# Optimization experiments

Hardware: AMD Instinct MI355X
Metric: run time of the kernel (lower is better)

Reference implementation:

```python
import jax, jax.numpy as jnp
import numpy as np

GAMMA = 1.0

def _rbf_mean(X, Y, gamma):
    x2 = jnp.sum(X * X, axis=1)  # [n]
    y2 = jnp.sum(Y * Y, axis=1)  # [m]
    d2 = x2[:, None] + y2[None, :] - 2.0 * (X @ Y.T)
    d2 = jnp.maximum(d2, 0.0)
    return jnp.mean(jnp.exp(-gamma * d2))

def setup_inputs() -> dict:
    key = jax.random.key(0)
    k1, k2 = jax.random.split(key)
    N = jax.random.normal(k1, (8192, 256), dtype=jnp.float32)
    R = jax.random.normal(k2, (8192, 256), dtype=jnp.float32)
    return {"N": N, "R": R}

def reference(N, R):
    xx = _rbf_mean(N, N, GAMMA)
    yy = _rbf_mean(R, R, GAMMA)
    xy = _rbf_mean(N, R, GAMMA)
    mmd = xx + yy - 2.0 * xy
    return jnp.sqrt(mmd)
```

## Files before the change

### kernel.cpp

```cpp
#include <hip/hip_runtime.h>
#include <math.h>

typedef float f32x4 __attribute__((ext_vector_type(4)));
typedef int   i32x4 __attribute__((ext_vector_type(4)));
typedef int   i32x8 __attribute__((ext_vector_type(8)));
typedef float f32x2 __attribute__((ext_vector_type(2)));

#define MTOT 16384
#define HALF 8192
#define KDIM 256
#define BM 128
#define NB (MTOT / BM)
#define NBLK (NB * (NB + 1) / 2)
#define NPART (NBLK * 4)

#define GLDS16(g, l) __builtin_amdgcn_global_load_lds(                      \
    (const __attribute__((address_space(1))) void*)(g),                     \
    (__attribute__((address_space(3))) void*)(l), 16, 0, 0)

__global__ __launch_bounds__(256) void convert_kernel(
    const float* __restrict__ Nmat, const float* __restrict__ Rmat,
    unsigned int* __restrict__ Z, float* __restrict__ x2) {
  const int lane = threadIdx.x & 63;
  const int wv = threadIdx.x >> 6;
  const int row = blockIdx.x * 4 + wv;
  const float* src = (row < HALF) ? (Nmat + (size_t)row * KDIM)
                                  : (Rmat + (size_t)(row - HALF) * KDIM);
  float4 v = *(const float4*)(src + lane * 4);
  int pk = __builtin_amdgcn_cvt_pk_fp8_f32(v.x, v.y, 0, false);
  pk = __builtin_amdgcn_cvt_pk_fp8_f32(v.z, v.w, pk, true);
  Z[(size_t)row * (KDIM / 4) + lane] = (unsigned int)pk;
  f32x2 d01 = __builtin_amdgcn_cvt_pk_f32_fp8(pk, false);
  f32x2 d23 = __builtin_amdgcn_cvt_pk_f32_fp8(pk, true);
  float sq = d01[0] * d01[0] + d01[1] * d01[1] + d23[0] * d23[0] + d23[1] * d23[1];
  #pragma unroll
  for (int off = 32; off; off >>= 1) sq += __shfl_down(sq, off);
  if (lane == 0) x2[row] = -0.5f * sq;
}

__global__ __launch_bounds__(256, 2) void mmd_gemm(
    const unsigned char* __restrict__ Z, const float* __restrict__ x2,
    float* __restrict__ partials) {
  const int t = (blockIdx.x & 7) * (NBLK / 8) + (blockIdx.x >> 3);
  const int u = NBLK - 1 - t;
  int rr = (int)((sqrtf(8.0f * (float)u + 1.0f) - 1.0f) * 0.5f);
  while (rr * (rr + 1) / 2 > u) --rr;
  while ((rr + 1) * (rr + 2) / 2 <= u) ++rr;
  const int bm = NB - 1 - rr;
  const int bn = bm + (t - (bm * NB - bm * (bm - 1) / 2));

  __shared__ __align__(16) unsigned char As[2][BM * 128];
  __shared__ __align__(16) unsigned char Bs[2][BM * 128];

  const int tid  = threadIdx.x;
  const int lane = tid & 63;
  const int wid  = tid >> 6;
  const int wm   = wid >> 1;
  const int wn   = wid & 1;

  const int lr = lane >> 3;
  const int ls = lane & 7;
  const int cofs = lr * KDIM + ((ls ^ lr) << 4);

  const int fr = lane & 15;
  const int fq = lane >> 4;
  const int key = fr & 7;
  const int slotL = ((2 * fq) ^ key) * 16;
  const int slotH = ((2 * fq + 1) ^ key) * 16;

  const unsigned char* Abase = Z + (size_t)bm * BM * KDIM;
  const unsigned char* Bbase = Z + (size_t)bn * BM * KDIM;

  auto STAGE = [&](int h) {
    #pragma unroll
    for (int tt = 0; tt < 4; ++tt) {
      int i = wid * 4 + tt;
      GLDS16(Abase + (size_t)i * 8 * KDIM + h * 128 + cofs, &As[h][i * 1024]);
      GLDS16(Bbase + (size_t)i * 8 * KDIM + h * 128 + cofs, &Bs[h][i * 1024]);
    }
  };

  STAGE(0);

  float xch[4];
  #pragma unroll
  for (int tn = 0; tn < 4; ++tn)
    xch[tn] = x2[bn * BM + wn * 64 + tn * 16 + fr];

  f32x4 acc[4][4];
  #pragma unroll
  for (int tm = 0; tm < 4; ++tm) {
    float4 xr = *(const float4*)(x2 + bm * BM + wm * 64 + tm * 16 + fq * 4);
    #pragma unroll
    for (int tn = 0; tn < 4; ++tn) {
      acc[tm][tn][0] = xr.x + xch[tn];
      acc[tm][tn][1] = xr.y + xch[tn];
      acc[tm][tn][2] = xr.z + xch[tn];
      acc[tm][tn][3] = xr.w + xch[tn];
    }
  }

  __syncthreads();
  STAGE(1);

  #pragma unroll
  for (int ks = 0; ks < 2; ++ks) {
    i32x8 bf[4];
    #pragma unroll
    for (int tn = 0; tn < 4; ++tn) {
      int row = wn * 64 + tn * 16 + fr;
      i32x4 lo = *(const i32x4*)(&Bs[ks][row * 128 + slotL]);
      i32x4 hi = *(const i32x4*)(&Bs[ks][row * 128 + slotH]);
      bf[tn] = __builtin_shufflevector(lo, hi, 0, 1, 2, 3, 4, 5, 6, 7);
    }
    #pragma unroll
    for (int tm = 0; tm < 4; ++tm) {
      int row = wm * 64 + tm * 16 + fr;
      i32x4 lo = *(const i32x4*)(&As[ks][row * 128 + slotL]);
      i32x4 hi = *(const i32x4*)(&As[ks][row * 128 + slotH]);
      i32x8 af = __builtin_shufflevector(lo, hi, 0, 1, 2, 3, 4, 5, 6, 7);
      #pragma unroll
      for (int tn = 0; tn < 4; ++tn)
        acc[tm][tn] = __builtin_amdgcn_mfma_scale_f32_16x16x128_f8f6f4(
            af, bf[tn], acc[tm][tn], 0, 0,
            0, 0x7F7F7F7F, 0, 0x7F7F7F7F);
    }
    if (ks == 0) __syncthreads();
  }

  float amax = -1e30f;
  #pragma unroll
  for (int tm = 0; tm < 4; ++tm)
    #pragma unroll
    for (int tn = 0; tn < 4; ++tn) {
      float m1 = fmaxf(fmaxf(acc[tm][tn][0], acc[tm][tn][1]), acc[tm][tn][2]);
      amax = fmaxf(fmaxf(amax, m1), acc[tm][tn][3]);
    }

  float partial = 0.f;
  if (__any(amax > -40.f)) {
    #pragma unroll
    for (int tm = 0; tm < 4; ++tm)
      #pragma unroll
      for (int tn = 0; tn < 4; ++tn)
        #pragma unroll
        for (int v = 0; v < 4; ++v) {
          float a = fminf(acc[tm][tn][v], 0.f);
          partial += exp2f(a * 2.885390082f);
        }
  }

  float wgt = ((bm < NB / 2) == (bn < NB / 2)) ? 1.f : -1.f;
  if (bm != bn) wgt *= 2.f;

  #pragma unroll
  for (int off = 32; off; off >>= 1) partial += __shfl_down(partial, off);
  if (lane == 0) partials[blockIdx.x * 4 + wid] = partial * wgt;
}

__global__ __launch_bounds__(1024) void finalize_kernel(
    const float* __restrict__ partials, float* __restrict__ out) {
  float s = 0.f;
  for (int i = threadIdx.x; i < NPART; i += 1024) s += partials[i];
  #pragma unroll
  for (int off = 32; off; off >>= 1) s += __shfl_down(s, off);
  __shared__ float ws[16];
  if ((threadIdx.x & 63) == 0) ws[threadIdx.x >> 6] = s;
  __syncthreads();
  if (threadIdx.x == 0) {
    float tot = 0.f;
    #pragma unroll
    for (int i = 0; i < 16; ++i) tot += ws[i];
    float mmd = tot / ((float)HALF * (float)HALF);
    out[0] = sqrtf(fmaxf(mmd, 0.f));
  }
}

extern "C" void kernel_launch(void* const* d_in, const int* in_sizes, int n_in,
                              void* d_out, int out_size, void* d_ws, size_t ws_size,
                              hipStream_t stream) {
  const float* Nmat = (const float*)d_in[0];
  const float* Rmat = (const float*)d_in[1];
  float* out = (float*)d_out;

  char* ws = (char*)d_ws;
  unsigned char* Z = (unsigned char*)ws;
  float* x2       = (float*)(ws + (size_t)MTOT * KDIM);
  float* partials = (float*)(ws + (size_t)MTOT * KDIM + MTOT * 4);

  convert_kernel<<<MTOT / 4, 256, 0, stream>>>(Nmat, Rmat, (unsigned int*)Z, x2);
  mmd_gemm<<<NBLK, 256, 0, stream>>>(Z, x2, partials);
  finalize_kernel<<<1, 1024, 0, stream>>>(partials, out);
}
```

Baseline: 125.6 us.

## Drop LDS staging and load MFMA fragments directly from global memory

The GEMM kernel no longer stages A/B tiles into shared memory through global_load_lds and barriers. Each wave now reads its fp8 fragments straight from global memory (relying on L1/L2 for reuse). Blocks grow to 512 threads in a 2x4 wave grid, each wave owning a 64x32 sub-tile. This removes LDS traffic and syncs and raises occupancy, but adds redundant global/L2 loads because fragments are no longer shared across waves through LDS.

```diff
diff --git a/kernel.cpp b/kernel.cpp
--- a/kernel.cpp
+++ b/kernel.cpp
@@ -12,11 +12,7 @@
 #define BM 128
 #define NB (MTOT / BM)
 #define NBLK (NB * (NB + 1) / 2)
-#define NPART (NBLK * 4)
-
-#define GLDS16(g, l) __builtin_amdgcn_global_load_lds(                      \
-    (const __attribute__((address_space(1))) void*)(g),                     \
-    (__attribute__((address_space(3))) void*)(l), 16, 0, 0)
+#define NPART (NBLK * 8)
 
 __global__ __launch_bounds__(256) void convert_kernel(
     const float* __restrict__ Nmat, const float* __restrict__ Rmat,
@@ -38,7 +34,7 @@
   if (lane == 0) x2[row] = -0.5f * sq;
 }
 
-__global__ __launch_bounds__(256, 2) void mmd_gemm(
+__global__ __launch_bounds__(512, 4) void mmd_gemm(
     const unsigned char* __restrict__ Z, const float* __restrict__ x2,
     float* __restrict__ partials) {
   const int t = (blockIdx.x & 7) * (NBLK / 8) + (blockIdx.x >> 3);
@@ -49,50 +45,30 @@
   const int bm = NB - 1 - rr;
   const int bn = bm + (t - (bm * NB - bm * (bm - 1) / 2));
 
-  __shared__ __align__(16) unsigned char As[2][BM * 128];
-  __shared__ __align__(16) unsigned char Bs[2][BM * 128];
-
-  const int tid  = threadIdx.x;
-  const int lane = tid & 63;
-  const int wid  = tid >> 6;
-  const int wm   = wid >> 1;
-  const int wn   = wid & 1;
-
-  const int lr = lane >> 3;
-  const int ls = lane & 7;
-  const int cofs = lr * KDIM + ((ls ^ lr) << 4);
+  const int lane = threadIdx.x & 63;
+  const int wid  = threadIdx.x >> 6;
+  const int wm   = wid >> 2;
+  const int wn   = wid & 3;
 
   const int fr = lane & 15;
   const int fq = lane >> 4;
-  const int key = fr & 7;
-  const int slotL = ((2 * fq) ^ key) * 16;
-  const int slotH = ((2 * fq + 1) ^ key) * 16;
 
-  const unsigned char* Abase = Z + (size_t)bm * BM * KDIM;
-  const unsigned char* Bbase = Z + (size_t)bn * BM * KDIM;
+  const unsigned char* Arow =
+      Z + (size_t)(bm * BM + wm * 64 + fr) * KDIM + fq * 32;
+  const unsigned char* Brow =
+      Z + (size_t)(bn * BM + wn * 32 + fr) * KDIM + fq * 32;
 
-  auto STAGE = [&](int h) {
-    #pragma unroll
-    for (int tt = 0; tt < 4; ++tt) {
-      int i = wid * 4 + tt;
-      GLDS16(Abase + (size_t)i * 8 * KDIM + h * 128 + cofs, &As[h][i * 1024]);
-      GLDS16(Bbase + (size_t)i * 8 * KDIM + h * 128 + cofs, &Bs[h][i * 1024]);
-    }
-  };
+  float xch[2];
+  #pragma unroll
+  for (int tn = 0; tn < 2; ++tn)
+    xch[tn] = x2[bn * BM + wn * 32 + tn * 16 + fr];
 
-  STAGE(0);
-
-  float xch[4];
-  #pragma unroll
-  for (int tn = 0; tn < 4; ++tn)
-    xch[tn] = x2[bn * BM + wn * 64 + tn * 16 + fr];
-
-  f32x4 acc[4][4];
+  f32x4 acc[4][2];
   #pragma unroll
   for (int tm = 0; tm < 4; ++tm) {
     float4 xr = *(const float4*)(x2 + bm * BM + wm * 64 + tm * 16 + fq * 4);
     #pragma unroll
-    for (int tn = 0; tn < 4; ++tn) {
+    for (int tn = 0; tn < 2; ++tn) {
       acc[tm][tn][0] = xr.x + xch[tn];
       acc[tm][tn][1] = xr.y + xch[tn];
       acc[tm][tn][2] = xr.z + xch[tn];
@@ -100,39 +76,35 @@
     }
   }
 
-  __syncthreads();
-  STAGE(1);
-
   #pragma unroll
   for (int ks = 0; ks < 2; ++ks) {
-    i32x8 bf[4];
+    i32x8 bf[2];
     #pragma unroll
-    for (int tn = 0; tn < 4; ++tn) {
-      int row = wn * 64 + tn * 16 + fr;
-      i32x4 lo = *(const i32x4*)(&Bs[ks][row * 128 + slotL]);
-      i32x4 hi = *(const i32x4*)(&Bs[ks][row * 128 + slotH]);
+    for (int tn = 0; tn < 2; ++tn) {
+      const unsigned char* p = Brow + (size_t)tn * 16 * KDIM + ks * 128;
+      i32x4 lo = *(const i32x4*)(p);
+      i32x4 hi = *(const i32x4*)(p + 16);
       bf[tn] = __builtin_shufflevector(lo, hi, 0, 1, 2, 3, 4, 5, 6, 7);
     }
     #pragma unroll
     for (int tm = 0; tm < 4; ++tm) {
-      int row = wm * 64 + tm * 16 + fr;
-      i32x4 lo = *(const i32x4*)(&As[ks][row * 128 + slotL]);
-      i32x4 hi = *(const i32x4*)(&As[ks][row * 128 + slotH]);
+      const unsigned char* p = Arow + (size_t)tm * 16 * KDIM + ks * 128;
+      i32x4 lo = *(const i32x4*)(p);
+      i32x4 hi = *(const i32x4*)(p + 16);
       i32x8 af = __builtin_shufflevector(lo, hi, 0, 1, 2, 3, 4, 5, 6, 7);
       #pragma unroll
-      for (int tn = 0; tn < 4; ++tn)
+      for (int tn = 0; tn < 2; ++tn)
         acc[tm][tn] = __builtin_amdgcn_mfma_scale_f32_16x16x128_f8f6f4(
             af, bf[tn], acc[tm][tn], 0, 0,
             0, 0x7F7F7F7F, 0, 0x7F7F7F7F);
     }
-    if (ks == 0) __syncthreads();
   }
 
   float amax = -1e30f;
   #pragma unroll
   for (int tm = 0; tm < 4; ++tm)
     #pragma unroll
-    for (int tn = 0; tn < 4; ++tn) {
+    for (int tn = 0; tn < 2; ++tn) {
       float m1 = fmaxf(fmaxf(acc[tm][tn][0], acc[tm][tn][1]), acc[tm][tn][2]);
       amax = fmaxf(fmaxf(amax, m1), acc[tm][tn][3]);
     }
@@ -142,7 +114,7 @@
     #pragma unroll
     for (int tm = 0; tm < 4; ++tm)
       #pragma unroll
-      for (int tn = 0; tn < 4; ++tn)
+      for (int tn = 0; tn < 2; ++tn)
         #pragma unroll
         for (int v = 0; v < 4; ++v) {
           float a = fminf(acc[tm][tn][v], 0.f);
@@ -155,7 +127,7 @@
 
   #pragma unroll
   for (int off = 32; off; off >>= 1) partial += __shfl_down(partial, off);
-  if (lane == 0) partials[blockIdx.x * 4 + wid] = partial * wgt;
+  if (lane == 0) partials[blockIdx.x * 8 + wid] = partial * wgt;
 }
 
 __global__ __launch_bounds__(1024) void finalize_kernel(
@@ -189,6 +161,6 @@
   float* partials = (float*)(ws + (size_t)MTOT * KDIM + MTOT * 4);
 
   convert_kernel<<<MTOT / 4, 256, 0, stream>>>(Nmat, Rmat, (unsigned int*)Z, x2);
-  mmd_gemm<<<NBLK, 256, 0, stream>>>(Z, x2, partials);
+  mmd_gemm<<<NBLK, 512, 0, stream>>>(Z, x2, partials);
   finalize_kernel<<<1, 1024, 0, stream>>>(partials, out);
 }
```

New measurement: 266.7 us. 2.12x slower.
